# Optimization experiments

Hardware: AMD Instinct MI355X
Metric: run time of the kernel (lower is better)

The kernel has to match this reference:

```python
import jax, jax.numpy as jnp
import numpy as np

B, S, H = 4, 4096, 1024
NUM_LEVELS, DECAY = 3, 0.8
D0, D1 = 512, 204  # int(1024*0.5), int(512*0.5*0.8)


def _xavier(key, shape):
    fan_in, fan_out = shape
    return jax.random.normal(key, shape, dtype=jnp.float32) * np.sqrt(2.0 / (fan_in + fan_out))


def setup_inputs() -> dict:
    key = jax.random.key(0)
    ks = jax.random.split(key, 8)
    return {
        "keys": jax.random.normal(ks[0], (B, S, H), dtype=jnp.float32),
        "values": jax.random.normal(ks[1], (B, S, H), dtype=jnp.float32),
        "importance": jax.random.uniform(ks[2], (B, S), dtype=jnp.float32),
        # encoder layers (stored as [in, out]; torch Linear applies x @ W.T + b)
        "We0": _xavier(ks[3], (H, D0)), "be0": jnp.zeros((D0,), jnp.float32),
        "We1": _xavier(ks[4], (D0, D1)), "be1": jnp.zeros((D1,), jnp.float32),
        # decoder layers
        "Wd0": _xavier(ks[5], (D0, H)), "bd0": jnp.zeros((H,), jnp.float32),
        "Wd1": _xavier(ks[6], (D1, D0)), "bd1": jnp.zeros((D0,), jnp.float32),
    }


def _level_sizes(n):
    sizes, remaining = [], n
    for i in range(NUM_LEVELS):
        if i == NUM_LEVELS - 1:
            sizes.append(remaining)
        else:
            sz = int(remaining * (1 - DECAY) * DECAY ** i)
            sizes.append(sz)
            remaining -= sz
    return sizes


def reference(keys, values, importance, We0, be0, We1, be1, Wd0, bd0, Wd1, bd1):
    n = B * S
    fk = keys.reshape(n, H)
    fv = values.reshape(n, H)
    sorted_idx = jnp.argsort(-importance.reshape(-1))  # descending importance
    sizes = _level_sizes(n)

    def chain(x, level):
        # encode 0..level-1 with ReLU, then decode level-1..0 with ReLU
        if level >= 1:
            x = jax.nn.relu(x @ We0 + be0)
        if level >= 2:
            x = jax.nn.relu(x @ We1 + be1)
            x = jax.nn.relu(x @ Wd1 + bd1)
        if level >= 1:
            x = jax.nn.relu(x @ Wd0 + bd0)
        return x

    ck = jnp.zeros_like(fk)
    cv = jnp.zeros_like(fv)
    start = 0
    for level, size in enumerate(sizes):
        if size <= 0:
            continue
        idx = jax.lax.dynamic_slice(sorted_idx, (start,), (size,))
        ck = ck.at[idx].set(chain(fk[idx], level))
        cv = cv.at[idx].set(chain(fv[idx], level))
        start += size
    return ck.reshape(B, S, H), cv.reshape(B, S, H)
```

## Files before the change

### kernel.cpp

```cpp
#include <hip/hip_runtime.h>

typedef __attribute__((ext_vector_type(8))) short short8;
typedef __attribute__((ext_vector_type(4))) float f32x4;

#define N_TOK   16384
#define HDIM    1024
#define OUT_OFF 16777216
#define M1ROWS  26216
#define M2ROWS  22022
#define L2ROW0  4194

__device__ __forceinline__ unsigned short f2bf(float f) {
  unsigned int u = __float_as_uint(f);
  u += 0x7FFFu + ((u >> 16) & 1u);
  return (unsigned short)(u >> 16);
}

__device__ __forceinline__ void rowmap(int r, int& is_v, int& rank) {
  if (r < 2097)       { is_v = 0; rank = 3276 + r; }
  else if (r < 4194)  { is_v = 1; rank = 1179 + r; }
  else if (r < 15205) { is_v = 0; rank = 1179 + r; }
  else                { is_v = 1; rank = r - 9832; }
}

__global__ __launch_bounds__(256) void rank_count(const float* __restrict__ imp,
                                                  int* __restrict__ counts) {
  __shared__ float sj[2048];
  const int i = blockIdx.x * 256 + threadIdx.x;
  const int jbase = blockIdx.y * 2048;
  const float vi = imp[i];
  for (int s = threadIdx.x; s < 2048; s += 256) sj[s] = imp[jbase + s];
  __syncthreads();
  int cnt = 0;
  #pragma unroll 8
  for (int s = 0; s < 2048; ++s) {
    float vj = sj[s];
    bool gt = vj > vi;
    bool eq = (vj == vi) && ((jbase + s) < i);
    cnt += (gt || eq) ? 1 : 0;
  }
  atomicAdd(&counts[i], cnt);
}

__global__ __launch_bounds__(256) void scatter_order(const int* __restrict__ counts,
                                                     int* __restrict__ order) {
  int i = blockIdx.x * 256 + threadIdx.x;
  order[counts[i]] = i;
}

__global__ __launch_bounds__(256) void wconv(unsigned short* __restrict__ dst,
                                             const float* __restrict__ src,
                                             int Nd, int Kd, int Nsrc, int Ksrc) {
  int idx = blockIdx.x * 256 + threadIdx.x;
  if (idx >= Nd * Kd) return;
  int n = idx / Kd, k = idx % Kd;
  float v = (n < Nsrc && k < Ksrc) ? src[k * Nsrc + n] : 0.f;
  dst[idx] = f2bf(v);
}

__global__ __launch_bounds__(256) void gather_rows(unsigned short* __restrict__ X,
                                                   const float* __restrict__ keys,
                                                   const float* __restrict__ values,
                                                   const int* __restrict__ order) {
  int r = blockIdx.x;
  int is_v, rank; rowmap(r, is_v, rank);
  int token = order[rank];
  const float* src = (is_v ? values : keys) + (size_t)token * HDIM;
  int c = threadIdx.x * 4;
  float4 f = *reinterpret_cast<const float4*>(src + c);
  ushort4 h;
  h.x = f2bf(f.x); h.y = f2bf(f.y); h.z = f2bf(f.z); h.w = f2bf(f.w);
  *reinterpret_cast<ushort4*>(X + (size_t)r * HDIM + c) = h;
}

__global__ __launch_bounds__(256) void copy_level0(float* __restrict__ out,
                                                   const float* __restrict__ keys,
                                                   const float* __restrict__ values,
                                                   const int* __restrict__ order) {
  int b = blockIdx.x;
  int is_v = b & 1, rank = b >> 1;
  int token = order[rank];
  const float* src = (is_v ? values : keys) + (size_t)token * HDIM;
  float* dst = out + (is_v ? OUT_OFF : 0) + (size_t)token * HDIM;
  int c = threadIdx.x * 4;
  *reinterpret_cast<float4*>(dst + c) = *reinterpret_cast<const float4*>(src + c);
}

#define GLDS16(g, l) __builtin_amdgcn_global_load_lds( \
    (const __attribute__((address_space(1))) void*)(g), \
    (__attribute__((address_space(3))) void*)(l), 16, 0, 0)

template<int MODE>
__global__ __launch_bounds__(512) void gemm_bias_relu(
    const unsigned short* __restrict__ A, int M, int K,
    const unsigned short* __restrict__ Bt, int N,
    const float* __restrict__ bias, int Nbias,
    unsigned short* __restrict__ Cbf, int ldc,
    float* __restrict__ outf, const int* __restrict__ order,
    int NP, int NC) {
  __shared__ __align__(16) unsigned short S[3][12288];
  const int bid = blockIdx.x;
  const int r8 = bid & 7;
  const int rest = bid >> 3;
  const int c8 = rest % NC;
  const int q8 = rest / NC;
  const int p8 = q8 * 8 + r8;
  if (p8 >= NP) return;
  const int row0 = p8 * 256, col0 = c8 * 128;

  const int tid = threadIdx.x;
  const int wave = tid >> 6, lane = tid & 63;
  const int lrow = lane >> 2;
  const int lk = (((lane & 3) ^ ((lane >> 3) & 3)) << 3);
  const int wr = (wave >> 1) * 64, wc = (wave & 1) * 64;

  const unsigned short* gp[3];
  int ldso[3];
  #pragma unroll
  for (int j = 0; j < 3; ++j) {
    const int g = wave * 3 + j;
    const bool isA = g < 16;
    int rr = isA ? (row0 + g * 16 + lrow) : (col0 + (g - 16) * 16 + lrow);
    const int lim = isA ? M : N;
    if (rr >= lim) rr = 0;
    gp[j] = (isA ? A : Bt) + (size_t)rr * K + lk;
    ldso[j] = g * 512;
  }

  f32x4 acc[4][4] = {};
  const int fr = lane & 15;
  const int qoff = (((lane >> 4) ^ ((fr >> 1) & 3)) << 3);

  const int nt = K >> 5;
  #pragma unroll
  for (int j = 0; j < 3; ++j) GLDS16(gp[j], S[0] + ldso[j]);
  #pragma unroll
  for (int j = 0; j < 3; ++j) GLDS16(gp[j] + 32, S[1] + ldso[j]);

  int cur = 0;
  for (int t = 0; t < nt; ++t) {
    if (t + 1 < nt) asm volatile("s_waitcnt vmcnt(3)" ::: "memory");
    else            asm volatile("s_waitcnt vmcnt(0)" ::: "memory");
    __builtin_amdgcn_s_barrier();
    __builtin_amdgcn_sched_barrier(0);
    const unsigned short* as = S[cur];
    const unsigned short* bs = S[cur] + 8192;
    short8 af[4], bfv[4];
    #pragma unroll
    for (int m = 0; m < 4; ++m)
      af[m] = *reinterpret_cast<const short8*>(as + (wr + m * 16 + fr) * 32 + qoff);
    #pragma unroll
    for (int n = 0; n < 4; ++n)
      bfv[n] = *reinterpret_cast<const short8*>(bs + (wc + n * 16 + fr) * 32 + qoff);
    if (t + 2 < nt) {
      const int k2 = (t + 2) << 5;
      int nb = cur + 2; if (nb >= 3) nb -= 3;
      #pragma unroll
      for (int j = 0; j < 3; ++j) GLDS16(gp[j] + k2, S[nb] + ldso[j]);
    }
    #pragma unroll
    for (int m = 0; m < 4; ++m)
      #pragma unroll
      for (int n = 0; n < 4; ++n)
        acc[m][n] = __builtin_amdgcn_mfma_f32_16x16x32_bf16(af[m], bfv[n], acc[m][n], 0, 0, 0);
    cur = (cur == 2) ? 0 : cur + 1;
  }

  const int orow = (lane >> 4) * 4;
  const int ocol = lane & 15;
  #pragma unroll
  for (int m = 0; m < 4; ++m) {
    #pragma unroll
    for (int n = 0; n < 4; ++n) {
      #pragma unroll
      for (int j = 0; j < 4; ++j) {
        int r = row0 + wr + m * 16 + orow + j;
        int c = col0 + wc + n * 16 + ocol;
        if (r < M && c < N) {
          float v = acc[m][n][j] + (c < Nbias ? bias[c] : 0.f);
          v = fmaxf(v, 0.f);
          if (MODE == 0) {
            Cbf[(size_t)r * ldc + c] = f2bf(v);
          } else {
            int iv, rk; rowmap(r, iv, rk);
            int token = order[rk];
            outf[(size_t)(iv ? OUT_OFF : 0) + (size_t)token * HDIM + c] = v;
          }
        }
      }
    }
  }
}

static inline int swz_grid(int NP, int NC) { return 8 * NC * ((NP + 7) / 8); }

extern "C" void kernel_launch(void* const* d_in, const int* in_sizes, int n_in,
                              void* d_out, int out_size, void* d_ws, size_t ws_size,
                              hipStream_t stream) {
  const float* keys   = (const float*)d_in[0];
  const float* values = (const float*)d_in[1];
  const float* imp    = (const float*)d_in[2];
  const float* We0    = (const float*)d_in[3];
  const float* be0    = (const float*)d_in[4];
  const float* We1    = (const float*)d_in[5];
  const float* be1    = (const float*)d_in[6];
  const float* Wd0    = (const float*)d_in[7];
  const float* bd0    = (const float*)d_in[8];
  const float* Wd1    = (const float*)d_in[9];
  const float* bd1    = (const float*)d_in[10];

  char* ws = (char*)d_ws;
  int* counts           = (int*)(ws);
  int* order            = (int*)(ws + 65536);
  unsigned short* We0T  = (unsigned short*)(ws + 131072);
  unsigned short* We1T  = (unsigned short*)(ws + 1179648);
  unsigned short* Wd1T  = (unsigned short*)(ws + 1409024);
  unsigned short* Wd0T  = (unsigned short*)(ws + 1638400);
  unsigned short* Y     = (unsigned short*)(ws + 2686976);
  unsigned short* Z     = (unsigned short*)(ws + 29532160);
  unsigned short* X = (unsigned short*)d_out;
  float* outf = (float*)d_out;

  hipMemsetAsync(counts, 0, 65536, stream);
  rank_count<<<dim3(64, 8), 256, 0, stream>>>(imp, counts);
  scatter_order<<<64, 256, 0, stream>>>(counts, order);

  wconv<<<2048, 256, 0, stream>>>(We0T, We0, 512, 1024, 512, 1024);
  wconv<<<448,  256, 0, stream>>>(We1T, We1, 224, 512, 204, 512);
  wconv<<<448,  256, 0, stream>>>(Wd1T, Wd1, 512, 224, 512, 204);
  wconv<<<2048, 256, 0, stream>>>(Wd0T, Wd0, 1024, 512, 1024, 512);

  gather_rows<<<M1ROWS, 256, 0, stream>>>(X, keys, values, order);

  gemm_bias_relu<0><<<swz_grid(103, 4), 512, 0, stream>>>(
      X, M1ROWS, 1024, We0T, 512, be0, 512, Y, 512, nullptr, nullptr, 103, 4);

  copy_level0<<<6552, 256, 0, stream>>>(outf, keys, values, order);

  gemm_bias_relu<0><<<swz_grid(87, 2), 512, 0, stream>>>(
      Y + (size_t)L2ROW0 * 512, M2ROWS, 512, We1T, 224, be1, 204, Z, 224,
      nullptr, nullptr, 87, 2);

  gemm_bias_relu<0><<<swz_grid(87, 4), 512, 0, stream>>>(
      Z, M2ROWS, 224, Wd1T, 512, bd1, 512, Y + (size_t)L2ROW0 * 512, 512,
      nullptr, nullptr, 87, 4);

  gemm_bias_relu<1><<<swz_grid(103, 8), 512, 0, stream>>>(
      Y, M1ROWS, 512, Wd0T, 1024, bd0, 1024, nullptr, 0, outf, order, 103, 8);
}
```

Baseline: 274.4 us.

## Double GEMM K-tile to 64 with split-phase prefetch and padded intermediate

The GEMM main loop now loads 64-wide K tiles instead of 32, with a new XOR swizzle across 8 chunks. Each tile is split into two half-steps whose MFMA groups run under raised wave priority, and the prefetch of the next-but-one tile is interleaved between them. Because K must now be a multiple of 64, the level-2 intermediate Z and the transposed Wd1 are padded from 224 to 256 columns, and Z is zeroed with a memset. The aim is fewer barriers per K step and better overlap of loads with MFMA, at the cost of doubled LDS use, which may cut occupancy despite launch_bounds(512,2), plus an extra memset.

```diff
diff --git a/kernel.cpp b/kernel.cpp
--- a/kernel.cpp
+++ b/kernel.cpp
@@ -91,83 +91,121 @@
     (__attribute__((address_space(3))) void*)(l), 16, 0, 0)
 
 template<int MODE>
-__global__ __launch_bounds__(512) void gemm_bias_relu(
+__global__ __launch_bounds__(512, 2) void gemm_bias_relu(
     const unsigned short* __restrict__ A, int M, int K,
     const unsigned short* __restrict__ Bt, int N,
     const float* __restrict__ bias, int Nbias,
     unsigned short* __restrict__ Cbf, int ldc,
     float* __restrict__ outf, const int* __restrict__ order,
     int NP, int NC) {
-  __shared__ __align__(16) unsigned short S[3][12288];
+  __shared__ __align__(16) unsigned short S[3][24576];
   const int bid = blockIdx.x;
-  const int r8 = bid & 7;
-  const int rest = bid >> 3;
-  const int c8 = rest % NC;
-  const int q8 = rest / NC;
+  const int r8 = bid & 7, rest = bid >> 3;
+  const int c8 = rest % NC, q8 = rest / NC;
   const int p8 = q8 * 8 + r8;
   if (p8 >= NP) return;
   const int row0 = p8 * 256, col0 = c8 * 128;
 
   const int tid = threadIdx.x;
   const int wave = tid >> 6, lane = tid & 63;
-  const int lrow = lane >> 2;
-  const int lk = (((lane & 3) ^ ((lane >> 3) & 3)) << 3);
+
+  const int srow = lane >> 3;
+  const int schunk = ((lane & 7) ^ srow) << 3;
+  const unsigned short* apg[4]; int aoff[4];
+  #pragma unroll
+  for (int j = 0; j < 4; ++j) {
+    int g = wave * 4 + j;
+    int rr = row0 + g * 8 + srow; if (rr >= M) rr = 0;
+    apg[j] = A + (size_t)rr * K + schunk;
+    aoff[j] = g * 512;
+  }
+  const unsigned short* bpg[2]; int boff[2];
+  #pragma unroll
+  for (int j = 0; j < 2; ++j) {
+    int g = wave * 2 + j;
+    int rr = col0 + g * 8 + srow; if (rr >= N) rr = 0;
+    bpg[j] = Bt + (size_t)rr * K + schunk;
+    boff[j] = 16384 + g * 512;
+  }
+
   const int wr = (wave >> 1) * 64, wc = (wave & 1) * 64;
-
-  const unsigned short* gp[3];
-  int ldso[3];
-  #pragma unroll
-  for (int j = 0; j < 3; ++j) {
-    const int g = wave * 3 + j;
-    const bool isA = g < 16;
-    int rr = isA ? (row0 + g * 16 + lrow) : (col0 + (g - 16) * 16 + lrow);
-    const int lim = isA ? M : N;
-    if (rr >= lim) rr = 0;
-    gp[j] = (isA ? A : Bt) + (size_t)rr * K + lk;
-    ldso[j] = g * 512;
-  }
+  const int fr = lane & 15, lch = lane >> 4;
+  const int q0 = ((lch ^ (fr & 7)) << 3);
+  const int q1 = (((4 | lch) ^ (fr & 7)) << 3);
 
   f32x4 acc[4][4] = {};
-  const int fr = lane & 15;
-  const int qoff = (((lane >> 4) ^ ((fr >> 1) & 3)) << 3);
-
-  const int nt = K >> 5;
-  #pragma unroll
-  for (int j = 0; j < 3; ++j) GLDS16(gp[j], S[0] + ldso[j]);
-  #pragma unroll
-  for (int j = 0; j < 3; ++j) GLDS16(gp[j] + 32, S[1] + ldso[j]);
-
-  int cur = 0;
+  const int nt = K >> 6;
+
+  #pragma unroll
+  for (int j = 0; j < 4; ++j) GLDS16(apg[j], S[0] + aoff[j]);
+  #pragma unroll
+  for (int j = 0; j < 2; ++j) GLDS16(bpg[j], S[0] + boff[j]);
+  #pragma unroll
+  for (int j = 0; j < 4; ++j) GLDS16(apg[j] + 64, S[1] + aoff[j]);
+  #pragma unroll
+  for (int j = 0; j < 2; ++j) GLDS16(bpg[j] + 64, S[1] + boff[j]);
+  asm volatile("s_waitcnt vmcnt(6)" ::: "memory");
+  __builtin_amdgcn_s_barrier();
+
+  int bufc = 0;
   for (int t = 0; t < nt; ++t) {
-    if (t + 1 < nt) asm volatile("s_waitcnt vmcnt(3)" ::: "memory");
-    else            asm volatile("s_waitcnt vmcnt(0)" ::: "memory");
-    __builtin_amdgcn_s_barrier();
+    const unsigned short* as = S[bufc];
+    const unsigned short* bs = S[bufc] + 16384;
+    const bool pf = (t + 2 < nt);
+    const int k2 = (t + 2) << 6;
+    int nb = bufc + 2; if (nb >= 3) nb -= 3;
+    short8 af[4], bf[4];
+    #pragma unroll
+    for (int m = 0; m < 4; ++m)
+      af[m] = *reinterpret_cast<const short8*>(as + (wr + m * 16 + fr) * 64 + q0);
+    #pragma unroll
+    for (int n = 0; n < 4; ++n)
+      bf[n] = *reinterpret_cast<const short8*>(bs + (wc + n * 16 + fr) * 64 + q0);
+    if (pf) {
+      GLDS16(apg[0] + k2, S[nb] + aoff[0]);
+      GLDS16(apg[1] + k2, S[nb] + aoff[1]);
+      GLDS16(bpg[0] + k2, S[nb] + boff[0]);
+    }
+    __builtin_amdgcn_s_barrier();
+    asm volatile("s_waitcnt lgkmcnt(0)" ::: "memory");
     __builtin_amdgcn_sched_barrier(0);
-    const unsigned short* as = S[cur];
-    const unsigned short* bs = S[cur] + 8192;
-    short8 af[4], bfv[4];
-    #pragma unroll
-    for (int m = 0; m < 4; ++m)
-      af[m] = *reinterpret_cast<const short8*>(as + (wr + m * 16 + fr) * 32 + qoff);
-    #pragma unroll
-    for (int n = 0; n < 4; ++n)
-      bfv[n] = *reinterpret_cast<const short8*>(bs + (wc + n * 16 + fr) * 32 + qoff);
-    if (t + 2 < nt) {
-      const int k2 = (t + 2) << 5;
-      int nb = cur + 2; if (nb >= 3) nb -= 3;
-      #pragma unroll
-      for (int j = 0; j < 3; ++j) GLDS16(gp[j] + k2, S[nb] + ldso[j]);
-    }
+    __builtin_amdgcn_s_setprio(1);
     #pragma unroll
     for (int m = 0; m < 4; ++m)
       #pragma unroll
       for (int n = 0; n < 4; ++n)
-        acc[m][n] = __builtin_amdgcn_mfma_f32_16x16x32_bf16(af[m], bfv[n], acc[m][n], 0, 0, 0);
-    cur = (cur == 2) ? 0 : cur + 1;
-  }
-
-  const int orow = (lane >> 4) * 4;
-  const int ocol = lane & 15;
+        acc[m][n] = __builtin_amdgcn_mfma_f32_16x16x32_bf16(af[m], bf[n], acc[m][n], 0, 0, 0);
+    __builtin_amdgcn_s_setprio(0);
+    __builtin_amdgcn_s_barrier();
+    #pragma unroll
+    for (int m = 0; m < 4; ++m)
+      af[m] = *reinterpret_cast<const short8*>(as + (wr + m * 16 + fr) * 64 + q1);
+    #pragma unroll
+    for (int n = 0; n < 4; ++n)
+      bf[n] = *reinterpret_cast<const short8*>(bs + (wc + n * 16 + fr) * 64 + q1);
+    if (pf) {
+      GLDS16(apg[2] + k2, S[nb] + aoff[2]);
+      GLDS16(apg[3] + k2, S[nb] + aoff[3]);
+      GLDS16(bpg[1] + k2, S[nb] + boff[1]);
+    }
+    __builtin_amdgcn_s_barrier();
+    asm volatile("s_waitcnt lgkmcnt(0)" ::: "memory");
+    __builtin_amdgcn_sched_barrier(0);
+    __builtin_amdgcn_s_setprio(1);
+    #pragma unroll
+    for (int m = 0; m < 4; ++m)
+      #pragma unroll
+      for (int n = 0; n < 4; ++n)
+        acc[m][n] = __builtin_amdgcn_mfma_f32_16x16x32_bf16(af[m], bf[n], acc[m][n], 0, 0, 0);
+    __builtin_amdgcn_s_setprio(0);
+    if (pf) asm volatile("s_waitcnt vmcnt(6)" ::: "memory");
+    else    asm volatile("s_waitcnt vmcnt(0)" ::: "memory");
+    __builtin_amdgcn_s_barrier();
+    bufc = (bufc == 2) ? 0 : bufc + 1;
+  }
+
+  const int orow = lch * 4;
+  const int ocol = fr;
   #pragma unroll
   for (int m = 0; m < 4; ++m) {
     #pragma unroll
@@ -215,19 +253,20 @@
   unsigned short* We0T  = (unsigned short*)(ws + 131072);
   unsigned short* We1T  = (unsigned short*)(ws + 1179648);
   unsigned short* Wd1T  = (unsigned short*)(ws + 1409024);
-  unsigned short* Wd0T  = (unsigned short*)(ws + 1638400);
-  unsigned short* Y     = (unsigned short*)(ws + 2686976);
-  unsigned short* Z     = (unsigned short*)(ws + 29532160);
+  unsigned short* Wd0T  = (unsigned short*)(ws + 1671168);
+  unsigned short* Y     = (unsigned short*)(ws + 2719744);
+  unsigned short* Z     = (unsigned short*)(ws + 29564928);
   unsigned short* X = (unsigned short*)d_out;
   float* outf = (float*)d_out;
 
   hipMemsetAsync(counts, 0, 65536, stream);
+  hipMemsetAsync(Z, 0, (size_t)22022 * 256 * 2, stream);
   rank_count<<<dim3(64, 8), 256, 0, stream>>>(imp, counts);
   scatter_order<<<64, 256, 0, stream>>>(counts, order);
 
   wconv<<<2048, 256, 0, stream>>>(We0T, We0, 512, 1024, 512, 1024);
   wconv<<<448,  256, 0, stream>>>(We1T, We1, 224, 512, 204, 512);
-  wconv<<<448,  256, 0, stream>>>(Wd1T, Wd1, 512, 224, 512, 204);
+  wconv<<<512,  256, 0, stream>>>(Wd1T, Wd1, 512, 256, 512, 204);
   wconv<<<2048, 256, 0, stream>>>(Wd0T, Wd0, 1024, 512, 1024, 512);
 
   gather_rows<<<M1ROWS, 256, 0, stream>>>(X, keys, values, order);
@@ -238,11 +277,11 @@
   copy_level0<<<6552, 256, 0, stream>>>(outf, keys, values, order);
 
   gemm_bias_relu<0><<<swz_grid(87, 2), 512, 0, stream>>>(
-      Y + (size_t)L2ROW0 * 512, M2ROWS, 512, We1T, 224, be1, 204, Z, 224,
+      Y + (size_t)L2ROW0 * 512, M2ROWS, 512, We1T, 224, be1, 204, Z, 256,
       nullptr, nullptr, 87, 2);
 
   gemm_bias_relu<0><<<swz_grid(87, 4), 512, 0, stream>>>(
-      Z, M2ROWS, 224, Wd1T, 512, bd1, 512, Y + (size_t)L2ROW0 * 512, 512,
+      Z, M2ROWS, 256, Wd1T, 512, bd1, 512, Y + (size_t)L2ROW0 * 512, 512,
       nullptr, nullptr, 87, 4);
 
   gemm_bias_relu<1><<<swz_grid(103, 8), 512, 0, stream>>>(
```

New measurement: 332.7 us. +21.3%, slower.

## Stage final GEMM epilogue through LDS for vectorized scattered row stores

Applied to the files above, without the earlier changes.

In the final decoder GEMM, the epilogue now writes the accumulator tiles into shared memory in four barrier-separated passes, then emits full 16-byte float4 stores per scattered output row. Previously each lane wrote single floats per element, with a rowmap and order lookup on every element. The gathered bf16 input buffer moves from the output buffer into workspace, so copy_level0 can run before the first GEMM without overwriting it. The cost is extra barriers and LDS reuse in the epilogue, and the bias read assumes all columns are in range (N equals Nbias).

```diff
diff --git a/kernel.cpp b/kernel.cpp
--- a/kernel.cpp
+++ b/kernel.cpp
@@ -168,24 +168,52 @@
 
   const int orow = (lane >> 4) * 4;
   const int ocol = lane & 15;
-  #pragma unroll
-  for (int m = 0; m < 4; ++m) {
-    #pragma unroll
-    for (int n = 0; n < 4; ++n) {
-      #pragma unroll
-      for (int j = 0; j < 4; ++j) {
-        int r = row0 + wr + m * 16 + orow + j;
-        int c = col0 + wc + n * 16 + ocol;
-        if (r < M && c < N) {
-          float v = acc[m][n][j] + (c < Nbias ? bias[c] : 0.f);
-          v = fmaxf(v, 0.f);
-          if (MODE == 0) {
-            Cbf[(size_t)r * ldc + c] = f2bf(v);
-          } else {
-            int iv, rk; rowmap(r, iv, rk);
-            int token = order[rk];
-            outf[(size_t)(iv ? OUT_OFF : 0) + (size_t)token * HDIM + c] = v;
+  if (MODE == 0) {
+    #pragma unroll
+    for (int m = 0; m < 4; ++m) {
+      #pragma unroll
+      for (int n = 0; n < 4; ++n) {
+        #pragma unroll
+        for (int j = 0; j < 4; ++j) {
+          int r = row0 + wr + m * 16 + orow + j;
+          int c = col0 + wc + n * 16 + ocol;
+          if (r < M && c < N) {
+            float v = acc[m][n][j] + (c < Nbias ? bias[c] : 0.f);
+            Cbf[(size_t)r * ldc + c] = f2bf(fmaxf(v, 0.f));
           }
+        }
+      }
+    }
+  } else {
+    float* Cl = (float*)S;
+    #pragma unroll 1
+    for (int p = 0; p < 4; ++p) {
+      __builtin_amdgcn_s_barrier();
+      if ((wave >> 1) == p) {
+        #pragma unroll
+        for (int m = 0; m < 4; ++m)
+          #pragma unroll
+          for (int n = 0; n < 4; ++n)
+            #pragma unroll
+            for (int j = 0; j < 4; ++j) {
+              int rr = m * 16 + orow + j;
+              int cc = wc + n * 16 + ocol;
+              float v = acc[m][n][j] + bias[col0 + cc];
+              Cl[rr * 136 + cc] = fmaxf(v, 0.f);
+            }
+      }
+      __builtin_amdgcn_s_barrier();
+      #pragma unroll
+      for (int u = 0; u < 4; ++u) {
+        int unit = tid + u * 512;
+        int rr = unit >> 5, ch = unit & 31;
+        int r = row0 + p * 64 + rr;
+        if (r < M) {
+          int iv, rk; rowmap(r, iv, rk);
+          int token = order[rk];
+          f32x4 v = *reinterpret_cast<const f32x4*>(Cl + rr * 136 + ch * 4);
+          *reinterpret_cast<f32x4*>(outf + (size_t)(iv ? OUT_OFF : 0) +
+                                    (size_t)token * HDIM + col0 + ch * 4) = v;
         }
       }
     }
@@ -218,7 +246,7 @@
   unsigned short* Wd0T  = (unsigned short*)(ws + 1638400);
   unsigned short* Y     = (unsigned short*)(ws + 2686976);
   unsigned short* Z     = (unsigned short*)(ws + 29532160);
-  unsigned short* X = (unsigned short*)d_out;
+  unsigned short* X     = (unsigned short*)(ws + 39398016);
   float* outf = (float*)d_out;
 
   hipMemsetAsync(counts, 0, 65536, stream);
@@ -231,11 +259,10 @@
   wconv<<<2048, 256, 0, stream>>>(Wd0T, Wd0, 1024, 512, 1024, 512);
 
   gather_rows<<<M1ROWS, 256, 0, stream>>>(X, keys, values, order);
+  copy_level0<<<6552, 256, 0, stream>>>(outf, keys, values, order);
 
   gemm_bias_relu<0><<<swz_grid(103, 4), 512, 0, stream>>>(
       X, M1ROWS, 1024, We0T, 512, be0, 512, Y, 512, nullptr, nullptr, 103, 4);
-
-  copy_level0<<<6552, 256, 0, stream>>>(outf, keys, values, order);
 
   gemm_bias_relu<0><<<swz_grid(87, 2), 512, 0, stream>>>(
       Y + (size_t)L2ROW0 * 512, M2ROWS, 512, We1T, 224, be1, 204, Z, 224,
```

After: 272.1 us. Within noise of the previous version (-0.8%).
